# Kernel optimization log

Hardware: AMD Instinct MI355X
Metric: run time of the kernel (lower is better)

Reference implementation:

```python
import jax, jax.numpy as jnp
import numpy as np

LOG2 = 0.6931471824645996  # float32 log(2), shifted-softplus offset

def ssp(v):
    return jax.nn.softplus(v) - LOG2

def setup_inputs() -> dict:
    key = jax.random.key(0)
    ks = jax.random.split(key, 8)
    B, A, N = 4, 512, 128
    n_in = n_factors = n_out = 256
    s_in = 1.0 / np.sqrt(n_in)
    s_f = 1.0 / np.sqrt(n_factors)
    return {
        "x": jax.random.normal(ks[0], (B, A, n_in), dtype=jnp.float32),
        "r_ij": jax.random.uniform(ks[1], (B, A, N), dtype=jnp.float32) * 5.0,
        "pairwise_mask": jnp.ones((B, A, N), dtype=jnp.float32),
        "in2f_w": jax.random.normal(ks[2], (n_in, n_factors), dtype=jnp.float32) * s_in,
        "in2f_b": jnp.zeros((n_factors,), dtype=jnp.float32),
        "f2out_w": jax.random.normal(ks[3], (n_factors, n_out), dtype=jnp.float32) * s_f,
        "f2out_b": jnp.zeros((n_out,), dtype=jnp.float32),
        "fw1": jax.random.normal(ks[4], (1, n_factors), dtype=jnp.float32),
        "fb1": jnp.zeros((n_factors,), dtype=jnp.float32),
        "fw2": jax.random.normal(ks[5], (n_factors, n_factors), dtype=jnp.float32) * s_f,
        "fb2": jnp.zeros((n_factors,), dtype=jnp.float32),
        "neighbors": jax.random.randint(ks[6], (B, A, N), 0, A, dtype=jnp.int64),
    }

def reference(x, r_ij, pairwise_mask, in2f_w, in2f_b, f2out_w, f2out_b,
              fw1, fb1, fw2, fb2, neighbors):
    # f_ij = r_ij.unsqueeze(-1); filter network: Dense+ssp -> Dense
    f_ij = r_ij[..., None]                                  # [B,A,N,1]
    W = ssp(f_ij @ fw1 + fb1) @ fw2 + fb2                   # [B,A,N,F]
    facts = x @ in2f_w + in2f_b                             # [B,A,F]
    B, A, N = neighbors.shape
    F = facts.shape[-1]
    # gather neighbor features along atom axis
    idx = neighbors.reshape(B, A * N)[..., None]            # [B,A*N,1]
    xj = jnp.take_along_axis(facts, idx, axis=1).reshape(B, A, N, F)
    xi = facts[:, :, None, :]                               # [B,A,1,F]
    y = xi * W * xj                                         # [B,A,N,F]
    y = ssp(y @ f2out_w + f2out_b)                          # [B,A,N,n_out]
    return y
```

## Files before the change

### kernel.cpp

```cpp
#include <hip/hip_runtime.h>
#include <hip/hip_bf16.h>
#include <stdint.h>

typedef unsigned short u16;

#define Adim 512
#define Ndim 128
#define Fdim 256
#define BA 2048

#define HS 264
#define XS 264

#define GRID 512
#define ITEMS 8

typedef __attribute__((ext_vector_type(8))) __bf16 bf16x8;
typedef __attribute__((ext_vector_type(4))) float f32x4;

__device__ __forceinline__ float bf2f(u16 u){
  uint32_t v = ((uint32_t)u) << 16;
  return __builtin_bit_cast(float, v);
}
__device__ __forceinline__ uint32_t cvtpk(float lo, float hi){
  uint32_t r;
  asm("v_cvt_pk_bf16_f32 %0, %1, %2" : "=v"(r) : "v"(lo), "v"(hi));
  return r;
}
__device__ __forceinline__ u16 f2bf(float f){ return (u16)cvtpk(f, f); }
__device__ __forceinline__ float ssp_f(float v){
  float m = fmaxf(v, 0.f);
  float e = __expf(-fabsf(v));
  return m + __logf(1.f + e) - 0.69314718f;
}

__global__ __launch_bounds__(256) void prep_kernel(
    const float* __restrict__ s0, u16* __restrict__ d0,
    const float* __restrict__ s1, u16* __restrict__ d1,
    const float* __restrict__ s2, u16* __restrict__ d2)
{
  __shared__ float tile[32][33];
  const float* src = (blockIdx.y == 0) ? s0 : (blockIdx.y == 1 ? s1 : s2);
  u16* dst = (blockIdx.y == 0) ? d0 : (blockIdx.y == 1 ? d1 : d2);
  int bx = (blockIdx.x & 7) * 32, by = (int)(blockIdx.x >> 3) * 32;
  int tx = threadIdx.x & 31, ty = threadIdx.x >> 5;
  #pragma unroll
  for (int r = 0; r < 4; r++)
    tile[ty + r*8][tx] = src[(size_t)(by + ty + r*8)*Fdim + bx + tx];
  __syncthreads();
  #pragma unroll
  for (int r = 0; r < 4; r++)
    dst[(size_t)(bx + ty + r*8)*Fdim + by + tx] = f2bf(tile[tx][ty + r*8]);
}

__global__ __launch_bounds__(256, 2) void facts_kernel(
    const float* __restrict__ x, const u16* __restrict__ wT,
    const float* __restrict__ bias, u16* __restrict__ facts)
{
  __shared__ __align__(16) u16 Xs[64*HS];
  const int tid = threadIdx.x;
  const int row0 = blockIdx.x * 64;

  #pragma unroll
  for (int i = 0; i < 16; i++){
    int id = i*256 + tid;
    int r = id >> 6, c4 = id & 63;
    float4 v = *(const float4*)(x + (size_t)(row0 + r)*Fdim + c4*4);
    uint2 q;
    q.x = cvtpk(v.x, v.y);
    q.y = cvtpk(v.z, v.w);
    *(uint2*)(Xs + r*HS + c4*4) = q;
  }
  __syncthreads();

  const int lane = tid & 63, wid = tid >> 6;
  const int wcol = wid * 64;
  const int l16 = lane & 15, quad = lane >> 4;

  f32x4 acc[4][4];
  #pragma unroll
  for (int mt = 0; mt < 4; mt++)
    #pragma unroll
    for (int ct = 0; ct < 4; ct++)
      acc[mt][ct] = (f32x4){0.f,0.f,0.f,0.f};

  const u16* wbase = wT + (size_t)(wcol + l16)*Fdim + quad*8;
  bf16x8 bb[2][4];
  #pragma unroll
  for (int ct = 0; ct < 4; ct++) bb[0][ct] = *(const bf16x8*)(wbase + ct*16*Fdim);

  for (int kk = 0; kk < 8; kk++){
    if (kk < 7){
      #pragma unroll
      for (int ct = 0; ct < 4; ct++)
        bb[(kk+1)&1][ct] = *(const bf16x8*)(wbase + ct*16*Fdim + (kk+1)*32);
    }
    bf16x8 af[4];
    #pragma unroll
    for (int mt = 0; mt < 4; mt++)
      af[mt] = *(const bf16x8*)(Xs + (mt*16 + l16)*HS + kk*32 + quad*8);
    #pragma unroll
    for (int mt = 0; mt < 4; mt++)
      #pragma unroll
      for (int ct = 0; ct < 4; ct++)
        acc[mt][ct] = __builtin_amdgcn_mfma_f32_16x16x32_bf16(af[mt], bb[kk&1][ct], acc[mt][ct], 0, 0, 0);
  }

  #pragma unroll
  for (int ct = 0; ct < 4; ct++){
    int f = wcol + ct*16 + l16;
    float bv = bias[f];
    #pragma unroll
    for (int mt = 0; mt < 4; mt++)
      #pragma unroll
      for (int i = 0; i < 4; i++){
        int m = mt*16 + quad*4 + i;
        facts[(size_t)(row0 + m)*Fdim + f] = f2bf(acc[mt][ct][i] + bv);
      }
  }
}

__global__ __launch_bounds__(512, 2) void fused_kernel(
    const float* __restrict__ r_ij, const u16* __restrict__ facts,
    const u16* __restrict__ fw2T, const u16* __restrict__ f2outT,
    const float* __restrict__ fw1, const float* __restrict__ fb1,
    const float* __restrict__ fb2, const float* __restrict__ f2out_b,
    const int* __restrict__ neighbors, float* __restrict__ out)
{
  __shared__ __align__(16) u16 Hs[64*HS];
  __shared__ __align__(16) u16 XJ[2][64*XS];
  __shared__ __align__(16) u16 Ys[64*HS];
  __shared__ int   nb_s[2][64];
  __shared__ float r_s[2][64];

  const int tid  = threadIdx.x;
  const int lane = tid & 63, wid = tid >> 6;
  const int l16  = lane & 15, quad = lane >> 4;
  const int wcol = wid * 32;
  const int g    = tid & 31;
  const int rsub = tid >> 5;

  float fw1v[8], fb1v[8];
  *(float4*)(fw1v)   = *(const float4*)(fw1 + g*8);
  *(float4*)(fw1v+4) = *(const float4*)(fw1 + g*8 + 4);
  *(float4*)(fb1v)   = *(const float4*)(fb1 + g*8);
  *(float4*)(fb1v+4) = *(const float4*)(fb1 + g*8 + 4);
  float fb2v[2], obv[2];
  #pragma unroll
  for (int ct = 0; ct < 2; ct++){
    int f = wcol + ct*16 + l16;
    fb2v[ct] = fb2[f];
    obv[ct]  = f2out_b[f];
  }

  const u16* w1base = fw2T   + (size_t)(wcol + l16)*Fdim + quad*8;
  const u16* w2base = f2outT + (size_t)(wcol + l16)*Fdim + quad*8;

  f32x4 accW[4][2], accZ[4][2];
  #pragma unroll
  for (int mt = 0; mt < 4; mt++)
    #pragma unroll
    for (int ct = 0; ct < 2; ct++){
      accW[mt][ct] = (f32x4){0.f,0.f,0.f,0.f};
      accZ[mt][ct] = (f32x4){0.f,0.f,0.f,0.f};
    }

  bf16x8 bw[4][2];

  {
    const int it0 = blockIdx.x;
    const int p0 = it0 >> 1, h0 = it0 & 1;
    if (tid < 64){
      nb_s[0][tid] = neighbors[(size_t)p0*Ndim + h0*64 + tid];
      r_s[0][tid]  = r_ij[(size_t)p0*Ndim + h0*64 + tid];
    }
  }
  __syncthreads();
  {
    const int it0 = blockIdx.x;
    const int p0 = it0 >> 1;
    const int bb0 = (p0 >> 9) << 9;
    float4 g0[4];
    #pragma unroll
    for (int i = 0; i < 4; i++){
      int row = i*16 + rsub;
      g0[i] = *(const float4*)(facts + ((size_t)(bb0 + nb_s[0][row]))*Fdim + g*8);
    }
    #pragma unroll
    for (int i = 0; i < 4; i++){
      int row = i*16 + rsub;
      float rv = r_s[0][row];
      float h[8];
      #pragma unroll
      for (int j = 0; j < 8; j++)
        h[j] = ssp_f(fmaf(rv, fw1v[j], fb1v[j]));
      uint4 pw;
      pw.x = cvtpk(h[0], h[1]);
      pw.y = cvtpk(h[2], h[3]);
      pw.z = cvtpk(h[4], h[5]);
      pw.w = cvtpk(h[6], h[7]);
      *(uint4*)(Hs + row*HS + g*8) = pw;
    }
    #pragma unroll
    for (int i = 0; i < 4; i++){
      int row = i*16 + rsub;
      *(float4*)(XJ[0] + row*XS + g*8) = g0[i];
    }
    if (tid < 64){
      const int it1 = GRID + blockIdx.x;
      const int p1 = it1 >> 1, h1 = it1 & 1;
      nb_s[1][tid] = neighbors[(size_t)p1*Ndim + h1*64 + tid];
      r_s[1][tid]  = r_ij[(size_t)p1*Ndim + h1*64 + tid];
    }
  }
  __syncthreads();

  for (int l = 0; l < ITEMS; l++){
    const int item = l*GRID + blockIdx.x;
    const int pair = item >> 1;
    const int half = item & 1;
    const int pa = l & 1, pb = (l+1) & 1;

    #pragma unroll
    for (int kk = 0; kk < 4; kk++)
      #pragma unroll
      for (int ct = 0; ct < 2; ct++)
        bw[kk][ct] = *(const bf16x8*)(w1base + ct*16*Fdim + kk*32);

    float4 gx[4];
    if (l + 1 < ITEMS){
      const int it1 = (l+1)*GRID + blockIdx.x;
      const int p1 = it1 >> 1;
      const int bb1 = (p1 >> 9) << 9;
      #pragma unroll
      for (int i = 0; i < 4; i++){
        int row = i*16 + rsub;
        gx[i] = *(const float4*)(facts + ((size_t)(bb1 + nb_s[pb][row]))*Fdim + g*8);
      }
    }

    int nb_nxt = 0; float r_nxt = 0.f;
    if (l + 2 < ITEMS && tid < 64){
      const int it2 = (l+2)*GRID + blockIdx.x;
      const int p2i = it2 >> 1, h2 = it2 & 1;
      nb_nxt = neighbors[(size_t)p2i*Ndim + h2*64 + tid];
      r_nxt  = r_ij[(size_t)p2i*Ndim + h2*64 + tid];
    }

    float xif[2];
    #pragma unroll
    for (int ct = 0; ct < 2; ct++)
      xif[ct] = bf2f(facts[(size_t)pair*Fdim + wcol + ct*16 + l16]);

    if (l > 0){
      const int pit = item - GRID;
      const int pp = pit >> 1, ph = pit & 1;
      size_t ob = ((size_t)pp * Ndim + ph*64) * Fdim;
      #pragma unroll
      for (int ct = 0; ct < 2; ct++){
        int f = wcol + ct*16 + l16;
        #pragma unroll
        for (int mt = 0; mt < 4; mt++){
          #pragma unroll
          for (int i = 0; i < 4; i++){
            int m = mt*16 + quad*4 + i;
            __builtin_nontemporal_store(ssp_f(accZ[mt][ct][i] + obv[ct]),
                                        out + ob + (size_t)m*Fdim + f);
            accZ[mt][ct][i] = 0.f;
          }
        }
      }
    }

    #pragma unroll
    for (int kk = 0; kk < 4; kk++){
      bf16x8 af[4];
      #pragma unroll
      for (int mt = 0; mt < 4; mt++)
        af[mt] = *(const bf16x8*)(Hs + (mt*16 + l16)*HS + kk*32 + quad*8);
      #pragma unroll
      for (int mt = 0; mt < 4; mt++)
        #pragma unroll
        for (int ct = 0; ct < 2; ct++)
          accW[mt][ct] = __builtin_amdgcn_mfma_f32_16x16x32_bf16(af[mt], bw[kk][ct], accW[mt][ct], 0, 0, 0);
    }
    if (l + 1 < ITEMS){
      #pragma unroll
      for (int i = 0; i < 4; i++){
        int row = i*16 + rsub;
        *(float4*)(XJ[pb] + row*XS + g*8) = gx[i];
      }
    }
    __builtin_amdgcn_sched_barrier(0);
    #pragma unroll
    for (int kk = 0; kk < 4; kk++)
      #pragma unroll
      for (int ct = 0; ct < 2; ct++)
        bw[kk][ct] = *(const bf16x8*)(w1base + ct*16*Fdim + (kk+4)*32);
    #pragma unroll
    for (int kk = 0; kk < 4; kk++){
      bf16x8 af[4];
      #pragma unroll
      for (int mt = 0; mt < 4; mt++)
        af[mt] = *(const bf16x8*)(Hs + (mt*16 + l16)*HS + (kk+4)*32 + quad*8);
      #pragma unroll
      for (int mt = 0; mt < 4; mt++)
        #pragma unroll
        for (int ct = 0; ct < 2; ct++)
          accW[mt][ct] = __builtin_amdgcn_mfma_f32_16x16x32_bf16(af[mt], bw[kk][ct], accW[mt][ct], 0, 0, 0);
    }
    __syncthreads();

    if (l + 2 < ITEMS && tid < 64){
      nb_s[pa][tid] = nb_nxt;
      r_s[pa][tid]  = r_nxt;
    }
    #pragma unroll
    for (int kk = 0; kk < 4; kk++)
      #pragma unroll
      for (int ct = 0; ct < 2; ct++)
        bw[kk][ct] = *(const bf16x8*)(w2base + ct*16*Fdim + kk*32);

    #pragma unroll
    for (int ct = 0; ct < 2; ct++){
      int f = wcol + ct*16 + l16;
      #pragma unroll
      for (int mt = 0; mt < 4; mt++){
        #pragma unroll
        for (int i = 0; i < 4; i++){
          int m = mt*16 + quad*4 + i;
          float wv = accW[mt][ct][i] + fb2v[ct];
          float y  = xif[ct] * wv * bf2f(XJ[pa][m*XS + f]);
          Ys[m*HS + f] = f2bf(y);
          accW[mt][ct][i] = 0.f;
        }
      }
    }

    if (l + 1 < ITEMS){
      #pragma unroll
      for (int i = 0; i < 4; i++){
        int row = i*16 + rsub;
        float rv = r_s[pb][row];
        float h[8];
        #pragma unroll
        for (int j = 0; j < 8; j++)
          h[j] = ssp_f(fmaf(rv, fw1v[j], fb1v[j]));
        uint4 pw;
        pw.x = cvtpk(h[0], h[1]);
        pw.y = cvtpk(h[2], h[3]);
        pw.z = cvtpk(h[4], h[5]);
        pw.w = cvtpk(h[6], h[7]);
        *(uint4*)(Hs + row*HS + g*8) = pw;
      }
    }
    __syncthreads();

    #pragma unroll
    for (int kk = 0; kk < 4; kk++){
      bf16x8 af[4];
      #pragma unroll
      for (int mt = 0; mt < 4; mt++)
        af[mt] = *(const bf16x8*)(Ys + (mt*16 + l16)*HS + kk*32 + quad*8);
      #pragma unroll
      for (int mt = 0; mt < 4; mt++)
        #pragma unroll
        for (int ct = 0; ct < 2; ct++)
          accZ[mt][ct] = __builtin_amdgcn_mfma_f32_16x16x32_bf16(af[mt], bw[kk][ct], accZ[mt][ct], 0, 0, 0);
    }
    __builtin_amdgcn_sched_barrier(0);
    #pragma unroll
    for (int kk = 0; kk < 4; kk++)
      #pragma unroll
      for (int ct = 0; ct < 2; ct++)
        bw[kk][ct] = *(const bf16x8*)(w2base + ct*16*Fdim + (kk+4)*32);
    #pragma unroll
    for (int kk = 0; kk < 4; kk++){
      bf16x8 af[4];
      #pragma unroll
      for (int mt = 0; mt < 4; mt++)
        af[mt] = *(const bf16x8*)(Ys + (mt*16 + l16)*HS + (kk+4)*32 + quad*8);
      #pragma unroll
      for (int mt = 0; mt < 4; mt++)
        #pragma unroll
        for (int ct = 0; ct < 2; ct++)
          accZ[mt][ct] = __builtin_amdgcn_mfma_f32_16x16x32_bf16(af[mt], bw[kk][ct], accZ[mt][ct], 0, 0, 0);
    }
  }

  {
    const int item = (ITEMS-1)*GRID + blockIdx.x;
    const int pp = item >> 1, ph = item & 1;
    size_t ob = ((size_t)pp * Ndim + ph*64) * Fdim;
    #pragma unroll
    for (int ct = 0; ct < 2; ct++){
      int f = wcol + ct*16 + l16;
      #pragma unroll
      for (int mt = 0; mt < 4; mt++){
        #pragma unroll
        for (int i = 0; i < 4; i++){
          int m = mt*16 + quad*4 + i;
          __builtin_nontemporal_store(ssp_f(accZ[mt][ct][i] + obv[ct]),
                                      out + ob + (size_t)m*Fdim + f);
        }
      }
    }
  }
}

extern "C" void kernel_launch(void* const* d_in, const int* in_sizes, int n_in,
                              void* d_out, int out_size, void* d_ws, size_t ws_size,
                              hipStream_t stream)
{
  const float* x        = (const float*)d_in[0];
  const float* r_ij     = (const float*)d_in[1];
  const float* in2f_w   = (const float*)d_in[3];
  const float* in2f_b   = (const float*)d_in[4];
  const float* f2out_w  = (const float*)d_in[5];
  const float* f2out_b  = (const float*)d_in[6];
  const float* fw1      = (const float*)d_in[7];
  const float* fb1      = (const float*)d_in[8];
  const float* fw2      = (const float*)d_in[9];
  const float* fb2      = (const float*)d_in[10];
  const int*   neighbors= (const int*)d_in[11];
  float* out = (float*)d_out;

  u16* facts  = (u16*)d_ws;
  u16* in2fT  = (u16*)((char*)d_ws + (1u<<20));
  u16* fw2T   = (u16*)((char*)d_ws + (1u<<20) + 1*(1u<<17));
  u16* f2outT = (u16*)((char*)d_ws + (1u<<20) + 2*(1u<<17));

  prep_kernel<<<dim3(64, 3), 256, 0, stream>>>(in2f_w, in2fT, fw2, fw2T, f2out_w, f2outT);
  facts_kernel<<<32, 256, 0, stream>>>(x, in2fT, in2f_b, facts);
  fused_kernel<<<GRID, 512, 0, stream>>>(r_ij, facts, fw2T, f2outT,
                                         fw1, fb1, fb2, f2out_b, neighbors, out);
}
```

Measured before the change: 491.5 us.

## Single-buffer XJ and index staging, reorder prefetch around second GEMM, software bf16 rounding

The double-buffered XJ, neighbor and r_ij shared arrays become single buffers, which frees LDS. The neighbor gather for the next item now starts after the first barrier and its results, along with the next H tile, are written after the second GEMM. This moves the gather latency behind the f2out MFMAs and lowers LDS pressure, which could help occupancy. The inline v_cvt_pk_bf16_f32 asm is replaced by software round-to-nearest-even bf16 conversion with per-element packing, which adds ALU instructions on the conversion paths.

```diff
diff --git a/kernel.cpp b/kernel.cpp
--- a/kernel.cpp
+++ b/kernel.cpp
@@ -18,16 +18,18 @@
 typedef __attribute__((ext_vector_type(8))) __bf16 bf16x8;
 typedef __attribute__((ext_vector_type(4))) float f32x4;
 
+union pack8 { bf16x8 v; u16 u[8]; };
+union pack4 { uint2 q; u16 u[4]; };
+
 __device__ __forceinline__ float bf2f(u16 u){
   uint32_t v = ((uint32_t)u) << 16;
   return __builtin_bit_cast(float, v);
 }
-__device__ __forceinline__ uint32_t cvtpk(float lo, float hi){
-  uint32_t r;
-  asm("v_cvt_pk_bf16_f32 %0, %1, %2" : "=v"(r) : "v"(lo), "v"(hi));
-  return r;
-}
-__device__ __forceinline__ u16 f2bf(float f){ return (u16)cvtpk(f, f); }
+__device__ __forceinline__ u16 f2bf(float f){
+  uint32_t v = __builtin_bit_cast(uint32_t, f);
+  v += 0x7fffu + ((v >> 16) & 1u);
+  return (u16)(v >> 16);
+}
 __device__ __forceinline__ float ssp_f(float v){
   float m = fmaxf(v, 0.f);
   float e = __expf(-fabsf(v));
@@ -66,10 +68,9 @@
     int id = i*256 + tid;
     int r = id >> 6, c4 = id & 63;
     float4 v = *(const float4*)(x + (size_t)(row0 + r)*Fdim + c4*4);
-    uint2 q;
-    q.x = cvtpk(v.x, v.y);
-    q.y = cvtpk(v.z, v.w);
-    *(uint2*)(Xs + r*HS + c4*4) = q;
+    pack4 p;
+    p.u[0] = f2bf(v.x); p.u[1] = f2bf(v.y); p.u[2] = f2bf(v.z); p.u[3] = f2bf(v.w);
+    *(uint2*)(Xs + r*HS + c4*4) = p.q;
   }
   __syncthreads();
 
@@ -128,10 +129,10 @@
     const int* __restrict__ neighbors, float* __restrict__ out)
 {
   __shared__ __align__(16) u16 Hs[64*HS];
-  __shared__ __align__(16) u16 XJ[2][64*XS];
+  __shared__ __align__(16) u16 XJ[64*XS];
   __shared__ __align__(16) u16 Ys[64*HS];
-  __shared__ int   nb_s[2][64];
-  __shared__ float r_s[2][64];
+  __shared__ int   nb_s[64];
+  __shared__ float r_s[64];
 
   const int tid  = threadIdx.x;
   const int lane = tid & 63, wid = tid >> 6;
@@ -171,8 +172,8 @@
     const int it0 = blockIdx.x;
     const int p0 = it0 >> 1, h0 = it0 & 1;
     if (tid < 64){
-      nb_s[0][tid] = neighbors[(size_t)p0*Ndim + h0*64 + tid];
-      r_s[0][tid]  = r_ij[(size_t)p0*Ndim + h0*64 + tid];
+      nb_s[tid] = neighbors[(size_t)p0*Ndim + h0*64 + tid];
+      r_s[tid]  = r_ij[(size_t)p0*Ndim + h0*64 + tid];
     }
   }
   __syncthreads();
@@ -184,33 +185,22 @@
     #pragma unroll
     for (int i = 0; i < 4; i++){
       int row = i*16 + rsub;
-      g0[i] = *(const float4*)(facts + ((size_t)(bb0 + nb_s[0][row]))*Fdim + g*8);
+      g0[i] = *(const float4*)(facts + ((size_t)(bb0 + nb_s[row]))*Fdim + g*8);
     }
     #pragma unroll
     for (int i = 0; i < 4; i++){
       int row = i*16 + rsub;
-      float rv = r_s[0][row];
-      float h[8];
+      float rv = r_s[row];
+      pack8 p;
       #pragma unroll
       for (int j = 0; j < 8; j++)
-        h[j] = ssp_f(fmaf(rv, fw1v[j], fb1v[j]));
-      uint4 pw;
-      pw.x = cvtpk(h[0], h[1]);
-      pw.y = cvtpk(h[2], h[3]);
-      pw.z = cvtpk(h[4], h[5]);
-      pw.w = cvtpk(h[6], h[7]);
-      *(uint4*)(Hs + row*HS + g*8) = pw;
+        p.u[j] = f2bf(ssp_f(fmaf(rv, fw1v[j], fb1v[j])));
+      *(bf16x8*)(Hs + row*HS + g*8) = p.v;
     }
     #pragma unroll
     for (int i = 0; i < 4; i++){
       int row = i*16 + rsub;
-      *(float4*)(XJ[0] + row*XS + g*8) = g0[i];
-    }
-    if (tid < 64){
-      const int it1 = GRID + blockIdx.x;
-      const int p1 = it1 >> 1, h1 = it1 & 1;
-      nb_s[1][tid] = neighbors[(size_t)p1*Ndim + h1*64 + tid];
-      r_s[1][tid]  = r_ij[(size_t)p1*Ndim + h1*64 + tid];
+      *(float4*)(XJ + row*XS + g*8) = g0[i];
     }
   }
   __syncthreads();
@@ -219,38 +209,24 @@
     const int item = l*GRID + blockIdx.x;
     const int pair = item >> 1;
     const int half = item & 1;
-    const int pa = l & 1, pb = (l+1) & 1;
+
+    int nb_nxt = 0; float r_nxt = 0.f;
+    if (l + 1 < ITEMS && tid < 64){
+      const int it1 = (l+1)*GRID + blockIdx.x;
+      const int p1 = it1 >> 1, h1 = it1 & 1;
+      nb_nxt = neighbors[(size_t)p1*Ndim + h1*64 + tid];
+      r_nxt  = r_ij[(size_t)p1*Ndim + h1*64 + tid];
+    }
+    float xif[2];
+    #pragma unroll
+    for (int ct = 0; ct < 2; ct++)
+      xif[ct] = bf2f(facts[(size_t)pair*Fdim + wcol + ct*16 + l16]);
 
     #pragma unroll
     for (int kk = 0; kk < 4; kk++)
       #pragma unroll
       for (int ct = 0; ct < 2; ct++)
         bw[kk][ct] = *(const bf16x8*)(w1base + ct*16*Fdim + kk*32);
-
-    float4 gx[4];
-    if (l + 1 < ITEMS){
-      const int it1 = (l+1)*GRID + blockIdx.x;
-      const int p1 = it1 >> 1;
-      const int bb1 = (p1 >> 9) << 9;
-      #pragma unroll
-      for (int i = 0; i < 4; i++){
-        int row = i*16 + rsub;
-        gx[i] = *(const float4*)(facts + ((size_t)(bb1 + nb_s[pb][row]))*Fdim + g*8);
-      }
-    }
-
-    int nb_nxt = 0; float r_nxt = 0.f;
-    if (l + 2 < ITEMS && tid < 64){
-      const int it2 = (l+2)*GRID + blockIdx.x;
-      const int p2i = it2 >> 1, h2 = it2 & 1;
-      nb_nxt = neighbors[(size_t)p2i*Ndim + h2*64 + tid];
-      r_nxt  = r_ij[(size_t)p2i*Ndim + h2*64 + tid];
-    }
-
-    float xif[2];
-    #pragma unroll
-    for (int ct = 0; ct < 2; ct++)
-      xif[ct] = bf2f(facts[(size_t)pair*Fdim + wcol + ct*16 + l16]);
 
     if (l > 0){
       const int pit = item - GRID;
@@ -284,13 +260,6 @@
         for (int ct = 0; ct < 2; ct++)
           accW[mt][ct] = __builtin_amdgcn_mfma_f32_16x16x32_bf16(af[mt], bw[kk][ct], accW[mt][ct], 0, 0, 0);
     }
-    if (l + 1 < ITEMS){
-      #pragma unroll
-      for (int i = 0; i < 4; i++){
-        int row = i*16 + rsub;
-        *(float4*)(XJ[pb] + row*XS + g*8) = gx[i];
-      }
-    }
     __builtin_amdgcn_sched_barrier(0);
     #pragma unroll
     for (int kk = 0; kk < 4; kk++)
@@ -309,17 +278,6 @@
         for (int ct = 0; ct < 2; ct++)
           accW[mt][ct] = __builtin_amdgcn_mfma_f32_16x16x32_bf16(af[mt], bw[kk][ct], accW[mt][ct], 0, 0, 0);
     }
-    __syncthreads();
-
-    if (l + 2 < ITEMS && tid < 64){
-      nb_s[pa][tid] = nb_nxt;
-      r_s[pa][tid]  = r_nxt;
-    }
-    #pragma unroll
-    for (int kk = 0; kk < 4; kk++)
-      #pragma unroll
-      for (int ct = 0; ct < 2; ct++)
-        bw[kk][ct] = *(const bf16x8*)(w2base + ct*16*Fdim + kk*32);
 
     #pragma unroll
     for (int ct = 0; ct < 2; ct++){
@@ -330,31 +288,36 @@
         for (int i = 0; i < 4; i++){
           int m = mt*16 + quad*4 + i;
           float wv = accW[mt][ct][i] + fb2v[ct];
-          float y  = xif[ct] * wv * bf2f(XJ[pa][m*XS + f]);
+          float y  = xif[ct] * wv * bf2f(XJ[m*XS + f]);
           Ys[m*HS + f] = f2bf(y);
           accW[mt][ct][i] = 0.f;
         }
       }
     }
 
+    if (l + 1 < ITEMS && tid < 64){
+      nb_s[tid] = nb_nxt;
+      r_s[tid]  = r_nxt;
+    }
+    __syncthreads();
+
+    #pragma unroll
+    for (int kk = 0; kk < 4; kk++)
+      #pragma unroll
+      for (int ct = 0; ct < 2; ct++)
+        bw[kk][ct] = *(const bf16x8*)(w2base + ct*16*Fdim + kk*32);
+
+    float4 gx[4];
     if (l + 1 < ITEMS){
+      const int it1 = (l+1)*GRID + blockIdx.x;
+      const int p1 = it1 >> 1;
+      const int bb1 = (p1 >> 9) << 9;
       #pragma unroll
       for (int i = 0; i < 4; i++){
         int row = i*16 + rsub;
-        float rv = r_s[pb][row];
-        float h[8];
-        #pragma unroll
-        for (int j = 0; j < 8; j++)
-          h[j] = ssp_f(fmaf(rv, fw1v[j], fb1v[j]));
-        uint4 pw;
-        pw.x = cvtpk(h[0], h[1]);
-        pw.y = cvtpk(h[2], h[3]);
-        pw.z = cvtpk(h[4], h[5]);
-        pw.w = cvtpk(h[6], h[7]);
-        *(uint4*)(Hs + row*HS + g*8) = pw;
-      }
-    }
-    __syncthreads();
+        gx[i] = *(const float4*)(facts + ((size_t)(bb1 + nb_s[row]))*Fdim + g*8);
+      }
+    }
 
     #pragma unroll
     for (int kk = 0; kk < 4; kk++){
@@ -386,6 +349,25 @@
         for (int ct = 0; ct < 2; ct++)
           accZ[mt][ct] = __builtin_amdgcn_mfma_f32_16x16x32_bf16(af[mt], bw[kk][ct], accZ[mt][ct], 0, 0, 0);
     }
+
+    if (l + 1 < ITEMS){
+      #pragma unroll
+      for (int i = 0; i < 4; i++){
+        int row = i*16 + rsub;
+        float rv = r_s[row];
+        pack8 p;
+        #pragma unroll
+        for (int j = 0; j < 8; j++)
+          p.u[j] = f2bf(ssp_f(fmaf(rv, fw1v[j], fb1v[j])));
+        *(bf16x8*)(Hs + row*HS + g*8) = p.v;
+      }
+      #pragma unroll
+      for (int i = 0; i < 4; i++){
+        int row = i*16 + rsub;
+        *(float4*)(XJ + row*XS + g*8) = gx[i];
+      }
+    }
+    __syncthreads();
   }
 
   {
```

Measured after the change: 608.9 us. 23.9% more time.
